# Kernel optimization log

Measured on AMD Instinct MI355X. Metric: run time of the kernel, lower is better.

Reference implementation:

```python
import jax, jax.numpy as jnp
import numpy as np

B, T, V, E, H = 4096, 128, 30, 256, 128

def setup_inputs() -> dict:
    key = jax.random.key(0)
    ks = jax.random.split(key, 12)
    inpt = jax.random.randint(ks[0], (B, T), 0, V, dtype=jnp.int32)
    h0 = jax.random.normal(ks[1], (B, H), dtype=jnp.float32)
    c0 = jax.random.normal(ks[2], (B, H), dtype=jnp.float32)
    mask_Y = jnp.ones((B, T), dtype=jnp.float32)
    s_e = 1.0
    s_l = 1.0 / np.sqrt(H)
    s_i = 1.0 / np.sqrt(E)
    emb = jax.random.normal(ks[3], (V, E), dtype=jnp.float32) * s_e
    W_ih = jax.random.normal(ks[4], (4 * H, E), dtype=jnp.float32) * s_i
    b_ih = jax.random.normal(ks[5], (4 * H,), dtype=jnp.float32) * s_i
    W_hh = jax.random.normal(ks[6], (4 * H, H), dtype=jnp.float32) * s_l
    b_hh = jax.random.normal(ks[7], (4 * H,), dtype=jnp.float32) * s_l
    W_lin = jax.random.normal(ks[8], (V, H), dtype=jnp.float32) * s_l
    b_lin = jax.random.normal(ks[9], (V,), dtype=jnp.float32) * s_l
    return {"inpt": inpt, "h0": h0, "c0": c0, "mask_Y": mask_Y, "beta": 1,
            "emb": emb, "W_ih": W_ih, "b_ih": b_ih, "W_hh": W_hh,
            "b_hh": b_hh, "W_lin": W_lin, "b_lin": b_lin}


def reference(inpt, h0, c0, mask_Y, beta, emb, W_ih, b_ih, W_hh, b_hh, W_lin, b_lin):
    # beta == 1 -> teacher forcing every step (u <= beta always), as in source.
    t_max = inpt.shape[1]
    # input tokens fed at steps t=0..t_max-2 are inpt[:, 0:t_max-1]
    x_emb = emb[inpt[:, :t_max - 1]]          # [B, T-1, E]
    xs = (jnp.swapaxes(x_emb, 0, 1),           # [T-1, B, E]
          inpt[:, 1:].T,                       # [T-1, B] true labels
          mask_Y[:, :t_max - 1].T)             # [T-1, B]

    def step(carry, xs_t):
        h, c = carry
        x, y, m = xs_t
        gates = x @ W_ih.T + b_ih + h @ W_hh.T + b_hh   # [B, 4H]
        i, f, g, o = jnp.split(gates, 4, axis=1)
        c2 = jax.nn.sigmoid(f) * c + jax.nn.sigmoid(i) * jnp.tanh(g)
        h2 = jax.nn.sigmoid(o) * jnp.tanh(c2)
        # -log(softmax(logits))[y] == -log_softmax(logits)[y]
        logp = jax.nn.log_softmax(h2 @ W_lin.T + b_lin, axis=1)  # [B, V]
        ce = -jnp.take_along_axis(logp, y[:, None], axis=1)[:, 0]
        return (h2, c2), jnp.sum(ce * m)

    _, step_losses = jax.lax.scan(step, (h0, c0), xs)
    return jnp.sum(step_losses) / jnp.sum(mask_Y)
```

## Files before the change

kernel.cpp:

```cpp
#include <hip/hip_runtime.h>


typedef __bf16 bf16x8 __attribute__((ext_vector_type(8)));
typedef float  f32x4  __attribute__((ext_vector_type(4)));

namespace {
constexpr int Bn = 4096, Tn = 128, Vn = 30, En = 256, Hn = 128, Gn = 512;
constexpr int WS_LOSS  = 0;
constexpr int WS_MASK  = 1;
constexpr int WS_CNT   = 2;
constexpr int WS_XPROJ = 16;
constexpr int WS_WF_F  = WS_XPROJ + Vn * Gn;
}

__device__ __forceinline__ float fexp2(float x) { return __builtin_amdgcn_exp2f(x); }
__device__ __forceinline__ float frcp(float x)  { return __builtin_amdgcn_rcpf(x); }
__device__ __forceinline__ float sigf(float x)  { return frcp(1.f + fexp2(x * -1.44269504f)); }
__device__ __forceinline__ float tanh_(float x) { return 1.f - 2.f * frcp(fexp2(x * 2.88539008f) + 1.f); }

__device__ __forceinline__ void lds_barrier() {
  __builtin_amdgcn_sched_barrier(0);
  asm volatile("s_waitcnt lgkmcnt(0)" ::: "memory");
  __builtin_amdgcn_s_barrier();
  __builtin_amdgcn_sched_barrier(0);
}

__global__ void k_setup(const float* __restrict__ emb, const float* __restrict__ W_ih,
                        const float* __restrict__ b_ih, const float* __restrict__ b_hh,
                        const float* __restrict__ W_hh, const float* __restrict__ W_lin,
                        float* __restrict__ ws) {
  const int bid = blockIdx.x, tid = threadIdx.x;
  if (bid < 60) {
    __shared__ __align__(16) float es[En];
    int v = bid >> 1;
    int j = ((bid & 1) << 8) + tid;
    es[tid] = emb[v * En + tid];
    __syncthreads();
    float a = b_ih[j] + b_hh[j];
    const float* wr = W_ih + j * En;
#pragma unroll 4
    for (int e = 0; e < En; e += 4) {
      float4 w = *(const float4*)(wr + e);
      float4 x = *(const float4*)(es + e);
      a += x.x * w.x + x.y * w.y + x.z * w.z + x.w * w.w;
    }
    ws[WS_XPROJ + v * Gn + (j & 127) * 4 + (j >> 7)] = a;
  } else if (bid < 92) {
    int fid = (bid - 60) * 256 + tid;
    int l = fid & 63, kt = (fid >> 6) & 3, g = (fid >> 8) & 3, w = fid >> 10;
    int n  = (g * 8 + w) * 16 + (l & 15);
    int k0 = kt * 32 + (l >> 4) * 8;
    const float* src = W_hh + n * Hn + k0;
    union { __bf16 h[8]; uint4 u; } pk;
#pragma unroll
    for (int j = 0; j < 8; ++j) pk.h[j] = (__bf16)src[j];
    __bf16* wf = (__bf16*)(ws + WS_WF_F);
    *(uint4*)(wf + fid * 8) = pk.u;
  } else {
    int fid = (bid - 92) * 256 + tid;
    if (fid < 3) ws[fid] = 0.f;
    int l = fid & 63, kt = (fid >> 6) & 3, n = fid >> 8;
    int col = n * 16 + (l & 15);
    int k0  = kt * 32 + (l >> 4) * 8;
    union { __bf16 h[8]; uint4 u; } pk;
#pragma unroll
    for (int j = 0; j < 8; ++j)
      pk.h[j] = (col < Vn) ? (__bf16)W_lin[col * Hn + k0 + j] : (__bf16)0.f;
    __bf16* wf = (__bf16*)(ws + WS_WF_F);
    *(uint4*)(wf + 65536 + fid * 8) = pk.u;
  }
}

__global__ __launch_bounds__(576, 1) void k_main(
    const int* __restrict__ inpt, const float* __restrict__ h0,
    const float* __restrict__ c0, const float* __restrict__ maskY,
    const float* __restrict__ b_lin, float* __restrict__ ws,
    float* __restrict__ out) {
  __shared__ __align__(16) __bf16 hbuf[2][16][136];
  __shared__ int   tokL[16 * 129];
  __shared__ float maskL[16 * 132];
  __shared__ __align__(16) float logits[16 * 36];
  __shared__ float red[2];

  const float4* X4 = (const float4*)(ws + WS_XPROJ);
  const __bf16* wf = (const __bf16*)(ws + WS_WF_F);
  const __bf16* wlf = wf + 65536;

  const int tid = threadIdx.x;
  const int w = tid >> 6, l = tid & 63, quad = l >> 4, lc = l & 15;
  const int row0 = blockIdx.x * 16;
  const int kh = w * 16 + lc;

  for (int idx = tid; idx < 16 * Tn; idx += 576) {
    int r = idx >> 7, t = idx & 127;
    tokL[r * 129 + t]  = inpt[(row0 + r) * Tn + t];
    maskL[r * 132 + t] = maskY[(row0 + r) * Tn + t];
  }
  for (int idx = tid; idx < 16 * Hn; idx += 576) {
    int r = idx >> 7, k = idx & 127;
    hbuf[0][r][k] = (__bf16)h0[(row0 + r) * Hn + k];
  }

  bf16x8 wreg[4][4];
  float  creg[4];
  float  bias0 = 0.f, bias1 = 0.f, mloc = 0.f;
  if (w < 8) {
#pragma unroll
    for (int g = 0; g < 4; ++g)
#pragma unroll
      for (int kt = 0; kt < 4; ++kt)
        wreg[g][kt] = __builtin_bit_cast(
            bf16x8, *(const uint4*)(wf + (((w * 4 + g) * 4 + kt) * 64 + l) * 8));
#pragma unroll
    for (int p = 0; p < 4; ++p)
      creg[p] = c0[(row0 + quad * 4 + p) * Hn + kh];
    if (w == 7) {
      float s = 0.f;
      const float4* m4 = (const float4*)(maskY + row0 * Tn);
#pragma unroll
      for (int i = 0; i < 8; ++i) s += m4[l + i * 64].x + m4[l + i * 64].y +
                                       m4[l + i * 64].z + m4[l + i * 64].w;
      mloc = s;
    }
  } else {
#pragma unroll
    for (int n = 0; n < 2; ++n)
#pragma unroll
      for (int kt = 0; kt < 4; ++kt)
        wreg[n][kt] = __builtin_bit_cast(
            bf16x8, *(const uint4*)(wlf + ((n * 4 + kt) * 64 + l) * 8));
    bias0 = b_lin[lc];
    bias1 = (lc < Vn - 16) ? b_lin[lc + 16] : -1e30f;
  }
  float ce_acc = 0.f;
  __syncthreads();

  float4 xv[4];
  if (w < 8) {
#pragma unroll
    for (int p = 0; p < 4; ++p)
      xv[p] = X4[tokL[(quad * 4 + p) * 129] * 128 + kh];
  }

  for (int t = 0; t < Tn; ++t) {
    const int par = t & 1;
    const __bf16* hc = &hbuf[par][0][0];
    __bf16*       hn = &hbuf[par ^ 1][0][0];

    if (w < 8) {
      if (t < Tn - 1) {
        bf16x8 af[4];
#pragma unroll
        for (int kt = 0; kt < 4; ++kt)
          af[kt] = __builtin_bit_cast(
              bf16x8, *(const uint4*)(hc + lc * 136 + kt * 32 + quad * 8));

        int tk[4];
#pragma unroll
        for (int p = 0; p < 4; ++p) tk[p] = tokL[(quad * 4 + p) * 129 + t + 1];

        f32x4 acc[4];
#pragma unroll
        for (int p = 0; p < 4; ++p) {
          acc[0][p] = xv[p].x; acc[1][p] = xv[p].y;
          acc[2][p] = xv[p].z; acc[3][p] = xv[p].w;
        }
#pragma unroll
        for (int g = 0; g < 4; ++g)
#pragma unroll
          for (int kt = 0; kt < 4; ++kt)
            acc[g] = __builtin_amdgcn_mfma_f32_16x16x32_bf16(af[kt], wreg[g][kt], acc[g], 0, 0, 0);

        float4 xn[4];
#pragma unroll
        for (int p = 0; p < 4; ++p) xn[p] = X4[tk[p] * 128 + kh];

#pragma unroll
        for (int p = 0; p < 4; ++p) {
          float c2 = sigf(acc[1][p]) * creg[p] + sigf(acc[0][p]) * tanh_(acc[2][p]);
          float h2 = sigf(acc[3][p]) * tanh_(c2);
          creg[p] = c2;
          hn[(quad * 4 + p) * 136 + kh] = (__bf16)h2;
          xv[p] = xn[p];
        }
      }
    } else if (t >= 1) {
      bf16x8 af[4];
#pragma unroll
      for (int kt = 0; kt < 4; ++kt)
        af[kt] = __builtin_bit_cast(
            bf16x8, *(const uint4*)(hc + lc * 136 + kt * 32 + quad * 8));
      f32x4 lacc[2] = {{bias0, bias0, bias0, bias0}, {bias1, bias1, bias1, bias1}};
#pragma unroll
      for (int kt = 0; kt < 4; ++kt) {
        lacc[0] = __builtin_amdgcn_mfma_f32_16x16x32_bf16(af[kt], wreg[0][kt], lacc[0], 0, 0, 0);
        lacc[1] = __builtin_amdgcn_mfma_f32_16x16x32_bf16(af[kt], wreg[1][kt], lacc[1], 0, 0, 0);
      }
#pragma unroll
      for (int p = 0; p < 4; ++p) {
        logits[(quad * 4 + p) * 36 + lc]      = lacc[0][p];
        logits[(quad * 4 + p) * 36 + 16 + lc] = lacc[1][p];
      }
      int row = l >> 2, j = l & 3;
      float4 v0 = *(const float4*)(logits + row * 36 + j * 8);
      float4 v1 = *(const float4*)(logits + row * 36 + j * 8 + 4);
      float m = fmaxf(fmaxf(fmaxf(v0.x, v0.y), fmaxf(v0.z, v0.w)),
                      fmaxf(fmaxf(v1.x, v1.y), fmaxf(v1.z, v1.w)));
      m = fmaxf(m, __shfl_xor(m, 1));
      m = fmaxf(m, __shfl_xor(m, 2));
      float e = fexp2((v0.x - m) * 1.44269504f) + fexp2((v0.y - m) * 1.44269504f) +
                fexp2((v0.z - m) * 1.44269504f) + fexp2((v0.w - m) * 1.44269504f) +
                fexp2((v1.x - m) * 1.44269504f) + fexp2((v1.y - m) * 1.44269504f) +
                fexp2((v1.z - m) * 1.44269504f) + fexp2((v1.w - m) * 1.44269504f);
      e += __shfl_xor(e, 1);
      e += __shfl_xor(e, 2);
      if (j == 0) {
        int   y  = tokL[row * 129 + t];
        float ly = logits[row * 36 + y];
        float ce = (m + __logf(e)) - ly;
        ce_acc += ce * maskL[row * 132 + t - 1];
      }
    }
    lds_barrier();
  }

  if (w == 7) {
#pragma unroll
    for (int off = 32; off > 0; off >>= 1) mloc += __shfl_down(mloc, off);
    if (l == 0) red[0] = mloc;
  }
  __syncthreads();
  if (w == 8) {
#pragma unroll
    for (int off = 32; off > 0; off >>= 1) ce_acc += __shfl_down(ce_acc, off);
    if (l == 0) {
      atomicAdd(ws + WS_LOSS, ce_acc);
      atomicAdd(ws + WS_MASK, red[0]);
      __threadfence();
      unsigned old = atomicAdd((unsigned*)(ws + WS_CNT), 1u);
      if (old == 255) {
        float lv = atomicAdd(ws + WS_LOSS, 0.f);
        float mv = atomicAdd(ws + WS_MASK, 0.f);
        out[0] = lv / mv;
      }
    }
  }
}

extern "C" void kernel_launch(void* const* d_in, const int* in_sizes, int n_in,
                              void* d_out, int out_size, void* d_ws, size_t ws_size,
                              hipStream_t stream) {
  const int*   inpt  = (const int*)  d_in[0];
  const float* h0    = (const float*)d_in[1];
  const float* c0    = (const float*)d_in[2];
  const float* maskY = (const float*)d_in[3];
  const float* emb   = (const float*)d_in[5];
  const float* W_ih  = (const float*)d_in[6];
  const float* b_ih  = (const float*)d_in[7];
  const float* W_hh  = (const float*)d_in[8];
  const float* b_hh  = (const float*)d_in[9];
  const float* W_lin = (const float*)d_in[10];
  const float* b_lin = (const float*)d_in[11];
  float* ws  = (float*)d_ws;
  float* out = (float*)d_out;

  hipLaunchKernelGGL(k_setup, dim3(94),  dim3(256), 0, stream,
                     emb, W_ih, b_ih, b_hh, W_hh, W_lin, ws);
  hipLaunchKernelGGL(k_main,  dim3(256), dim3(576), 0, stream,
                     inpt, h0, c0, maskY, b_lin, ws, out);
}
```

Measured before the change: 229.3 us.

## Drop dedicated output wave; spread logits and softmax over gate waves, pipelined

Removes the ninth wave that computed output logits and softmax. Waves 0-1 now compute the two halves of the logits with MFMA, reusing the h fragments they already loaded for the gate matmul. Waves 2-3 run the log-softmax and cross-entropy one step later from a double-buffered logits array, so the reduction overlaps the next recurrence step. This shrinks the block to 512 threads and shortens the per-step critical path, but adds one extra loop iteration and puts the logit work on two of the gate waves.

```diff
diff --git a/kernel.cpp b/kernel.cpp
--- a/kernel.cpp
+++ b/kernel.cpp
@@ -71,7 +71,7 @@
   }
 }
 
-__global__ __launch_bounds__(576, 1) void k_main(
+__global__ __launch_bounds__(512, 1) void k_main(
     const int* __restrict__ inpt, const float* __restrict__ h0,
     const float* __restrict__ c0, const float* __restrict__ maskY,
     const float* __restrict__ b_lin, float* __restrict__ ws,
@@ -79,11 +79,11 @@
   __shared__ __align__(16) __bf16 hbuf[2][16][136];
   __shared__ int   tokL[16 * 129];
   __shared__ float maskL[16 * 132];
-  __shared__ __align__(16) float logits[16 * 36];
+  __shared__ __align__(16) float logitsL[2][16 * 36];
   __shared__ float red[2];
 
   const float4* X4 = (const float4*)(ws + WS_XPROJ);
-  const __bf16* wf = (const __bf16*)(ws + WS_WF_F);
+  const __bf16* wf  = (const __bf16*)(ws + WS_WF_F);
   const __bf16* wlf = wf + 65536;
 
   const int tid = threadIdx.x;
@@ -91,134 +91,127 @@
   const int row0 = blockIdx.x * 16;
   const int kh = w * 16 + lc;
 
-  for (int idx = tid; idx < 16 * Tn; idx += 576) {
+  for (int idx = tid; idx < 16 * Tn; idx += 512) {
     int r = idx >> 7, t = idx & 127;
     tokL[r * 129 + t]  = inpt[(row0 + r) * Tn + t];
     maskL[r * 132 + t] = maskY[(row0 + r) * Tn + t];
   }
-  for (int idx = tid; idx < 16 * Hn; idx += 576) {
+  for (int idx = tid; idx < 16 * Hn; idx += 512) {
     int r = idx >> 7, k = idx & 127;
     hbuf[0][r][k] = (__bf16)h0[(row0 + r) * Hn + k];
   }
 
   bf16x8 wreg[4][4];
+  bf16x8 wlin[4];
   float  creg[4];
-  float  bias0 = 0.f, bias1 = 0.f, mloc = 0.f;
-  if (w < 8) {
-#pragma unroll
-    for (int g = 0; g < 4; ++g)
-#pragma unroll
-      for (int kt = 0; kt < 4; ++kt)
-        wreg[g][kt] = __builtin_bit_cast(
-            bf16x8, *(const uint4*)(wf + (((w * 4 + g) * 4 + kt) * 64 + l) * 8));
-#pragma unroll
-    for (int p = 0; p < 4; ++p)
-      creg[p] = c0[(row0 + quad * 4 + p) * Hn + kh];
-    if (w == 7) {
-      float s = 0.f;
-      const float4* m4 = (const float4*)(maskY + row0 * Tn);
-#pragma unroll
-      for (int i = 0; i < 8; ++i) s += m4[l + i * 64].x + m4[l + i * 64].y +
-                                       m4[l + i * 64].z + m4[l + i * 64].w;
-      mloc = s;
-    }
-  } else {
-#pragma unroll
-    for (int n = 0; n < 2; ++n)
-#pragma unroll
-      for (int kt = 0; kt < 4; ++kt)
-        wreg[n][kt] = __builtin_bit_cast(
-            bf16x8, *(const uint4*)(wlf + ((n * 4 + kt) * 64 + l) * 8));
-    bias0 = b_lin[lc];
-    bias1 = (lc < Vn - 16) ? b_lin[lc + 16] : -1e30f;
-  }
-  float ce_acc = 0.f;
+  float  blin = 0.f, mloc = 0.f, ce_acc = 0.f;
+
+#pragma unroll
+  for (int g = 0; g < 4; ++g)
+#pragma unroll
+    for (int kt = 0; kt < 4; ++kt)
+      wreg[g][kt] = __builtin_bit_cast(
+          bf16x8, *(const uint4*)(wf + (((w * 4 + g) * 4 + kt) * 64 + l) * 8));
+#pragma unroll
+  for (int p = 0; p < 4; ++p)
+    creg[p] = c0[(row0 + quad * 4 + p) * Hn + kh];
+
+  if (w == 7) {
+    float s = 0.f;
+    const float4* m4 = (const float4*)(maskY + row0 * Tn);
+#pragma unroll
+    for (int i = 0; i < 8; ++i) s += m4[l + i * 64].x + m4[l + i * 64].y +
+                                     m4[l + i * 64].z + m4[l + i * 64].w;
+    mloc = s;
+  }
+  if (w < 2) {
+#pragma unroll
+    for (int kt = 0; kt < 4; ++kt)
+      wlin[kt] = __builtin_bit_cast(
+          bf16x8, *(const uint4*)(wlf + ((w * 4 + kt) * 64 + l) * 8));
+    blin = (w == 0) ? b_lin[lc] : ((lc < Vn - 16) ? b_lin[16 + lc] : -1e30f);
+  }
   __syncthreads();
 
   float4 xv[4];
-  if (w < 8) {
-#pragma unroll
-    for (int p = 0; p < 4; ++p)
-      xv[p] = X4[tokL[(quad * 4 + p) * 129] * 128 + kh];
-  }
-
-  for (int t = 0; t < Tn; ++t) {
+#pragma unroll
+  for (int p = 0; p < 4; ++p)
+    xv[p] = X4[tokL[(quad * 4 + p) * 129] * 128 + kh];
+
+  for (int t = 0; t <= Tn; ++t) {
     const int par = t & 1;
     const __bf16* hc = &hbuf[par][0][0];
     __bf16*       hn = &hbuf[par ^ 1][0][0];
 
-    if (w < 8) {
-      if (t < Tn - 1) {
-        bf16x8 af[4];
-#pragma unroll
-        for (int kt = 0; kt < 4; ++kt)
-          af[kt] = __builtin_bit_cast(
-              bf16x8, *(const uint4*)(hc + lc * 136 + kt * 32 + quad * 8));
-
-        int tk[4];
-#pragma unroll
-        for (int p = 0; p < 4; ++p) tk[p] = tokL[(quad * 4 + p) * 129 + t + 1];
-
-        f32x4 acc[4];
-#pragma unroll
-        for (int p = 0; p < 4; ++p) {
-          acc[0][p] = xv[p].x; acc[1][p] = xv[p].y;
-          acc[2][p] = xv[p].z; acc[3][p] = xv[p].w;
-        }
-#pragma unroll
-        for (int g = 0; g < 4; ++g)
-#pragma unroll
-          for (int kt = 0; kt < 4; ++kt)
-            acc[g] = __builtin_amdgcn_mfma_f32_16x16x32_bf16(af[kt], wreg[g][kt], acc[g], 0, 0, 0);
-
-        float4 xn[4];
-#pragma unroll
-        for (int p = 0; p < 4; ++p) xn[p] = X4[tk[p] * 128 + kh];
-
-#pragma unroll
-        for (int p = 0; p < 4; ++p) {
-          float c2 = sigf(acc[1][p]) * creg[p] + sigf(acc[0][p]) * tanh_(acc[2][p]);
-          float h2 = sigf(acc[3][p]) * tanh_(c2);
-          creg[p] = c2;
-          hn[(quad * 4 + p) * 136 + kh] = (__bf16)h2;
-          xv[p] = xn[p];
-        }
-      }
-    } else if (t >= 1) {
-      bf16x8 af[4];
+    bf16x8 af[4];
+    const bool have_af = (t < Tn - 1) || (w < 2 && t < Tn);
+    if (have_af) {
 #pragma unroll
       for (int kt = 0; kt < 4; ++kt)
         af[kt] = __builtin_bit_cast(
             bf16x8, *(const uint4*)(hc + lc * 136 + kt * 32 + quad * 8));
-      f32x4 lacc[2] = {{bias0, bias0, bias0, bias0}, {bias1, bias1, bias1, bias1}};
-#pragma unroll
-      for (int kt = 0; kt < 4; ++kt) {
-        lacc[0] = __builtin_amdgcn_mfma_f32_16x16x32_bf16(af[kt], wreg[0][kt], lacc[0], 0, 0, 0);
-        lacc[1] = __builtin_amdgcn_mfma_f32_16x16x32_bf16(af[kt], wreg[1][kt], lacc[1], 0, 0, 0);
-      }
+    }
+
+    if (t < Tn - 1) {
+      int tk[4];
+#pragma unroll
+      for (int p = 0; p < 4; ++p) tk[p] = tokL[(quad * 4 + p) * 129 + t + 1];
+
+      f32x4 acc[4];
 #pragma unroll
       for (int p = 0; p < 4; ++p) {
-        logits[(quad * 4 + p) * 36 + lc]      = lacc[0][p];
-        logits[(quad * 4 + p) * 36 + 16 + lc] = lacc[1][p];
-      }
-      int row = l >> 2, j = l & 3;
-      float4 v0 = *(const float4*)(logits + row * 36 + j * 8);
-      float4 v1 = *(const float4*)(logits + row * 36 + j * 8 + 4);
-      float m = fmaxf(fmaxf(fmaxf(v0.x, v0.y), fmaxf(v0.z, v0.w)),
-                      fmaxf(fmaxf(v1.x, v1.y), fmaxf(v1.z, v1.w)));
+        acc[0][p] = xv[p].x; acc[1][p] = xv[p].y;
+        acc[2][p] = xv[p].z; acc[3][p] = xv[p].w;
+      }
+#pragma unroll
+      for (int g = 0; g < 4; ++g)
+#pragma unroll
+        for (int kt = 0; kt < 4; ++kt)
+          acc[g] = __builtin_amdgcn_mfma_f32_16x16x32_bf16(af[kt], wreg[g][kt], acc[g], 0, 0, 0);
+
+      float4 xn[4];
+#pragma unroll
+      for (int p = 0; p < 4; ++p) xn[p] = X4[tk[p] * 128 + kh];
+
+#pragma unroll
+      for (int p = 0; p < 4; ++p) {
+        float c2 = sigf(acc[1][p]) * creg[p] + sigf(acc[0][p]) * tanh_(acc[2][p]);
+        float h2 = sigf(acc[3][p]) * tanh_(c2);
+        creg[p] = c2;
+        hn[(quad * 4 + p) * 136 + kh] = (__bf16)h2;
+        xv[p] = xn[p];
+      }
+    }
+
+    if (w < 2 && t >= 1 && t < Tn) {
+      f32x4 lacc = {blin, blin, blin, blin};
+#pragma unroll
+      for (int kt = 0; kt < 4; ++kt)
+        lacc = __builtin_amdgcn_mfma_f32_16x16x32_bf16(af[kt], wlin[kt], lacc, 0, 0, 0);
+#pragma unroll
+      for (int p = 0; p < 4; ++p)
+        logitsL[par][(quad * 4 + p) * 36 + kh] = lacc[p];
+    }
+
+    if ((w == 2 || w == 3) && t >= 2) {
+      int srow = (w - 2) * 8 + (l >> 3);
+      int j = l & 7;
+      const float* Lr = &logitsL[par ^ 1][srow * 36];
+      float4 v = *(const float4*)(Lr + j * 4);
+      float m = fmaxf(fmaxf(v.x, v.y), fmaxf(v.z, v.w));
       m = fmaxf(m, __shfl_xor(m, 1));
       m = fmaxf(m, __shfl_xor(m, 2));
-      float e = fexp2((v0.x - m) * 1.44269504f) + fexp2((v0.y - m) * 1.44269504f) +
-                fexp2((v0.z - m) * 1.44269504f) + fexp2((v0.w - m) * 1.44269504f) +
-                fexp2((v1.x - m) * 1.44269504f) + fexp2((v1.y - m) * 1.44269504f) +
-                fexp2((v1.z - m) * 1.44269504f) + fexp2((v1.w - m) * 1.44269504f);
+      m = fmaxf(m, __shfl_xor(m, 4));
+      float e = fexp2((v.x - m) * 1.44269504f) + fexp2((v.y - m) * 1.44269504f) +
+                fexp2((v.z - m) * 1.44269504f) + fexp2((v.w - m) * 1.44269504f);
       e += __shfl_xor(e, 1);
       e += __shfl_xor(e, 2);
+      e += __shfl_xor(e, 4);
       if (j == 0) {
-        int   y  = tokL[row * 129 + t];
-        float ly = logits[row * 36 + y];
+        int   y  = tokL[srow * 129 + t - 1];
+        float ly = Lr[y];
         float ce = (m + __logf(e)) - ly;
-        ce_acc += ce * maskL[row * 132 + t - 1];
+        ce_acc += ce * maskL[srow * 132 + t - 2];
       }
     }
     lds_barrier();
@@ -229,12 +222,17 @@
     for (int off = 32; off > 0; off >>= 1) mloc += __shfl_down(mloc, off);
     if (l == 0) red[0] = mloc;
   }
+  if (w == 3) {
+#pragma unroll
+    for (int off = 32; off > 0; off >>= 1) ce_acc += __shfl_down(ce_acc, off);
+    if (l == 0) red[1] = ce_acc;
+  }
   __syncthreads();
-  if (w == 8) {
+  if (w == 2) {
 #pragma unroll
     for (int off = 32; off > 0; off >>= 1) ce_acc += __shfl_down(ce_acc, off);
     if (l == 0) {
-      atomicAdd(ws + WS_LOSS, ce_acc);
+      atomicAdd(ws + WS_LOSS, ce_acc + red[1]);
       atomicAdd(ws + WS_MASK, red[0]);
       __threadfence();
       unsigned old = atomicAdd((unsigned*)(ws + WS_CNT), 1u);
@@ -266,6 +264,6 @@
 
   hipLaunchKernelGGL(k_setup, dim3(94),  dim3(256), 0, stream,
                      emb, W_ih, b_ih, b_hh, W_hh, W_lin, ws);
-  hipLaunchKernelGGL(k_main,  dim3(256), dim3(576), 0, stream,
+  hipLaunchKernelGGL(k_main,  dim3(256), dim3(512), 0, stream,
                      inpt, h0, c0, maskY, b_lin, ws, out);
 }
```

After: 234.1 us. 1.02x slower.
